# Kernel tuning notes

Hardware: AMD Instinct MI355X
Metric: run time of the kernel (lower is better)

The kernel has to match this reference:

```python
import jax, jax.numpy as jnp
import numpy as np

NUM_CAPSULE = 32
DIM_CAPSULE = 16
ROUTINGS = 3
EPS = 1e-7  # K.epsilon()


def squash(x, axis=-1):
    s2 = jnp.sum(jnp.square(x), axis=axis, keepdims=True) + EPS
    scale = jnp.sqrt(s2) / (0.5 + s2)
    return scale * x


def setup_inputs() -> dict:
    key = jax.random.key(0)
    kx, kw = jax.random.split(key)
    x = jax.random.normal(kx, (128, 2048, 128), dtype=jnp.float32)
    # glorot-uniform-scale init for (in_dim, num_capsule*dim_capsule)
    fan_in, fan_out = 128, NUM_CAPSULE * DIM_CAPSULE
    limit = np.sqrt(6.0 / (fan_in + fan_out)).astype(np.float32)
    kernel = jax.random.uniform(kw, (fan_in, fan_out), dtype=jnp.float32,
                                minval=-limit, maxval=limit)
    return {"x": x, "kernel": kernel}


def reference(x, kernel):
    B, N, _ = x.shape
    # share_weights=True: 1x1 conv1d == matmul over input_dim_capsule
    hat = jnp.einsum('bnd,dm->bnm', x, kernel)            # (B, N, C*D)
    hat = hat.reshape(B, N, NUM_CAPSULE, DIM_CAPSULE)
    hat = jnp.transpose(hat, (0, 2, 1, 3))                # (B, C, N, D)
    b = jnp.zeros(hat.shape[:3], dtype=hat.dtype)         # (B, C, N)
    o = None
    for i in range(ROUTINGS):
        c = jax.nn.softmax(b, axis=1)                     # softmax over output capsules
        o = squash(jnp.einsum('bcn,bcnd->bcd', c, hat))   # (B, C, D)
        if i < ROUTINGS - 1:
            b = jnp.einsum('bcd,bcnd->bcn', o, hat)       # agreement (replaces b, per code)
    return o
```

## Files before the change

### kernel.cpp

```cpp
#include <hip/hip_runtime.h>
#include <hip/hip_bf16.h>


#define SEQ 2048
#define KD  128

typedef __attribute__((ext_vector_type(8))) short bf16x8;
typedef __attribute__((ext_vector_type(4))) float f32x4;

__device__ __forceinline__ short f2bf(float f) {
  unsigned u = __float_as_uint(f);
  u = u + 0x7fffu + ((u >> 16) & 1u);
  return (short)(u >> 16);
}
__device__ __forceinline__ int swz(int row) {
  return ((row & 7) << 4) ^ ((row & 24) << 2);
}

__global__ __launch_bounds__(256) void prep_k(const float* __restrict__ x,
                                              short* __restrict__ xs,
                                              float* __restrict__ S) {
  int blk = blockIdx.x;
  int t = threadIdx.x, oct = t & 15, rsub = t >> 4;
  size_t row0 = (size_t)blk * 128;
  char* dst = (char*)xs + (size_t)blk * 32768;
  float sac[8] = {0.f,0.f,0.f,0.f,0.f,0.f,0.f,0.f};
  #pragma unroll
  for (int sub = 0; sub < 8; ++sub) {
    int r = sub * 16 + rsub;
    const float* gp = x + (row0 + r) * KD + oct * 8;
    float4 f0 = *(const float4*)gp, f1 = *(const float4*)(gp + 4);
    bf16x8 v; short* vp = (short*)&v;
    vp[0] = f2bf(f0.x); vp[1] = f2bf(f0.y); vp[2] = f2bf(f0.z); vp[3] = f2bf(f0.w);
    vp[4] = f2bf(f1.x); vp[5] = f2bf(f1.y); vp[6] = f2bf(f1.z); vp[7] = f2bf(f1.w);
    sac[0] += f0.x; sac[1] += f0.y; sac[2] += f0.z; sac[3] += f0.w;
    sac[4] += f1.x; sac[5] += f1.y; sac[6] += f1.z; sac[7] += f1.w;
    *(bf16x8*)(dst + ((r * 256 + oct * 16) ^ swz(r))) = v;
  }
  __shared__ float red[2048];
  float4* rp = (float4*)&red[rsub * 128 + oct * 8];
  rp[0] = make_float4(sac[0], sac[1], sac[2], sac[3]);
  rp[1] = make_float4(sac[4], sac[5], sac[6], sac[7]);
  __syncthreads();
  if (t < 128) {
    float s = 0.f;
    #pragma unroll
    for (int i = 0; i < 16; ++i) s += red[i * 128 + t];
    atomicAdd(&S[(blk >> 4) * KD + t], s);
  }
}

__global__ __launch_bounds__(64) void small_k(const float* __restrict__ W,
                                              const float* __restrict__ S,
                                              const float* __restrict__ yp,
                                              short* __restrict__ wt,
                                              float* __restrict__ out,
                                              int mode) {
  int b = blockIdx.x >> 5, c = blockIdx.x & 31;
  int l = threadIdx.x, d = l & 15, kg = l >> 4;
  const float* Wc = W + c * 16;
  float s = 0.f;
  if (mode == 0) {
    const float* Sp = S + b * KD;
    #pragma unroll 8
    for (int i = 0; i < 32; ++i) { int k = kg * 32 + i; s += Sp[k] * Wc[k * 512 + d]; }
    s *= (1.f / 32.f);
  } else {
    const float* y0 = yp + (size_t)b * 4 * 4096 + c * KD;
    #pragma unroll 8
    for (int i = 0; i < 32; ++i) {
      int k = kg * 32 + i;
      float yv = y0[k] + y0[4096 + k] + y0[8192 + k] + y0[12288 + k];
      s += yv * Wc[k * 512 + d];
    }
  }
  s += __shfl_xor(s, 16); s += __shfl_xor(s, 32);
  float s2 = s * s;
  s2 += __shfl_xor(s2, 1); s2 += __shfl_xor(s2, 2);
  s2 += __shfl_xor(s2, 4); s2 += __shfl_xor(s2, 8);
  s2 += 1e-7f;
  float o = (sqrtf(s2) / (0.5f + s2)) * s;
  if (mode == 2) { if (l < 16) out[(size_t)b * 512 + c * 16 + l] = o; return; }
  __shared__ float olds[16];
  if (l < 16) olds[l] = o;
  __syncthreads();
  #pragma unroll
  for (int h = 0; h < 2; ++h) {
    int k = l + h * 64;
    float acc = 0.f;
    #pragma unroll
    for (int dd = 0; dd < 16; ++dd) acc += olds[dd] * Wc[k * 512 + dd];
    wt[((size_t)b * 32 + c) * KD + k] = f2bf(acc);
  }
}

__global__ __launch_bounds__(256, 2) void pass_k(const short* __restrict__ xs,
                                                 const short* __restrict__ wt,
                                                 float* __restrict__ yout) {
  __shared__ char ldsbuf[49152];
  char* lx  = ldsbuf;
  char* lw  = ldsbuf + 32768;
  char* lcn = ldsbuf + 40960;
  float* yred = (float*)ldsbuf;

  int b = blockIdx.x >> 2;
  int t = threadIdx.x;
  int wv = t >> 6, lane = t & 63, l15 = lane & 15, lg = lane >> 4;

  {
    int e = t * 16, c = e >> 7, k = e & 127;
    const short* gw = wt + (size_t)b * 4096 + e;
    bf16x8 w0 = *(const bf16x8*)gw;
    bf16x8 w1 = *(const bf16x8*)(gw + 8);
    int sw = (c & 7) << 4;
    *(bf16x8*)(lw + ((c * 256 + k * 2) ^ sw)) = w0;
    *(bf16x8*)(lw + ((c * 256 + (k + 8) * 2) ^ sw)) = w1;
  }

  f32x4 zz = {0.f, 0.f, 0.f, 0.f};
  f32x4 yacc[2][8];
  #pragma unroll
  for (int i = 0; i < 2; ++i)
    #pragma unroll
    for (int j = 0; j < 8; ++j) yacc[i][j] = zz;

  for (int chunk = 0; chunk < 4; ++chunk) {
    {
      const char* gs = (const char*)xs + ((size_t)blockIdx.x * 4 + chunk) * 32768;
      #pragma unroll
      for (int sub = 0; sub < 8; ++sub) {
        int off = sub * 4096 + t * 16;
        *(bf16x8*)(lx + off) = *(const bf16x8*)(gs + off);
      }
    }
    __syncthreads();

    f32x4 sc[2][2];
    sc[0][0] = zz; sc[0][1] = zz; sc[1][0] = zz; sc[1][1] = zz;
    #pragma unroll
    for (int ks = 0; ks < 4; ++ks) {
      bf16x8 a[2], bw[2];
      #pragma unroll
      for (int mi = 0; mi < 2; ++mi) {
        int row = wv * 32 + mi * 16 + l15;
        a[mi] = *(const bf16x8*)(lx + ((row * 256 + ks * 64 + lg * 16) ^ swz(row)));
      }
      #pragma unroll
      for (int ct = 0; ct < 2; ++ct) {
        int cc = ct * 16 + l15;
        bw[ct] = *(const bf16x8*)(lw + ((cc * 256 + ks * 64 + lg * 16) ^ ((cc & 7) << 4)));
      }
      #pragma unroll
      for (int mi = 0; mi < 2; ++mi)
        #pragma unroll
        for (int ct = 0; ct < 2; ++ct)
          sc[mi][ct] = __builtin_amdgcn_mfma_f32_16x16x32_bf16(a[mi], bw[ct], sc[mi][ct], 0, 0, 0);
    }

    #pragma unroll
    for (int mi = 0; mi < 2; ++mi) {
      #pragma unroll
      for (int r = 0; r < 4; ++r) {
        float v0 = sc[mi][0][r], v1 = sc[mi][1][r];
        float mx = fmaxf(v0, v1);
        mx = fmaxf(mx, __shfl_xor(mx, 1));
        mx = fmaxf(mx, __shfl_xor(mx, 2));
        mx = fmaxf(mx, __shfl_xor(mx, 4));
        mx = fmaxf(mx, __shfl_xor(mx, 8));
        float e0 = __expf(v0 - mx), e1 = __expf(v1 - mx);
        float sm = e0 + e1;
        sm += __shfl_xor(sm, 1); sm += __shfl_xor(sm, 2);
        sm += __shfl_xor(sm, 4); sm += __shfl_xor(sm, 8);
        float inv = 1.f / sm;
        int row = wv * 32 + mi * 16 + lg * 4 + r;
        int c0 = l15, c1 = 16 + l15;
        *(short*)(lcn + ((c0 * 256 + row * 2) ^ ((c0 & 7) << 4))) = f2bf(e0 * inv);
        *(short*)(lcn + ((c1 * 256 + row * 2) ^ ((c1 & 7) << 4))) = f2bf(e1 * inv);
      }
    }
    __syncthreads();

    {
      bf16x8 a2[2];
      #pragma unroll
      for (int m2 = 0; m2 < 2; ++m2) {
        int cc = m2 * 16 + l15;
        a2[m2] = *(const bf16x8*)(lcn + ((cc * 256 + wv * 64 + lg * 16) ^ ((cc & 7) << 4)));
      }
      #pragma unroll
      for (int nt = 0; nt < 8; ++nt) {
        bf16x8 bx;
        short* bp = (short*)&bx;
        int col = nt * 16 + l15;
        int rbase = wv * 32 + lg * 8;
        #pragma unroll
        for (int j = 0; j < 8; ++j) {
          int row = rbase + j;
          bp[j] = *(const short*)(lx + ((row * 256 + col * 2) ^ swz(row)));
        }
        yacc[0][nt] = __builtin_amdgcn_mfma_f32_16x16x32_bf16(a2[0], bx, yacc[0][nt], 0, 0, 0);
        yacc[1][nt] = __builtin_amdgcn_mfma_f32_16x16x32_bf16(a2[1], bx, yacc[1][nt], 0, 0, 0);
      }
    }
    __syncthreads();
  }

  #pragma unroll 1
  for (int round = 0; round < 4; ++round) {
    if (wv == round) {
      #pragma unroll
      for (int m2 = 0; m2 < 2; ++m2)
        #pragma unroll
        for (int nt = 0; nt < 8; ++nt)
          #pragma unroll
          for (int r = 0; r < 4; ++r) {
            int cc = m2 * 16 + lg * 4 + r;
            int kk = nt * 16 + l15;
            if (round == 0) yred[cc * 128 + kk]  = yacc[m2][nt][r];
            else            yred[cc * 128 + kk] += yacc[m2][nt][r];
          }
    }
    __syncthreads();
  }
  float* yo = yout + (size_t)blockIdx.x * 4096;
  #pragma unroll
  for (int i = 0; i < 16; ++i) yo[i * 256 + t] = yred[i * 256 + t];
}

extern "C" void kernel_launch(void* const* d_in, const int* in_sizes, int n_in,
                              void* d_out, int out_size, void* d_ws, size_t ws_size,
                              hipStream_t stream) {
  const float* x = (const float*)d_in[0];
  const float* W = (const float*)d_in[1];
  float* out = (float*)d_out;
  char* ws = (char*)d_ws;
  float* S  = (float*)ws;
  float* y1 = (float*)(ws + 65536);
  float* y2 = (float*)(ws + 65536 + 8388608);
  short* wt = (short*)(ws + 65536 + 16777216);
  short* xs = (short*)(ws + 20971520);

  hipMemsetAsync(S, 0, 65536, stream);

  prep_k <<<dim3(2048), dim3(256), 0, stream>>>(x, xs, S);
  small_k<<<dim3(4096), dim3(64), 0, stream>>>(W, S, nullptr, wt, nullptr, 0);
  pass_k <<<dim3(512), dim3(256), 0, stream>>>(xs, wt, y1);
  small_k<<<dim3(4096), dim3(64), 0, stream>>>(W, nullptr, y1, wt, nullptr, 1);
  pass_k <<<dim3(512), dim3(256), 0, stream>>>(xs, wt, y2);
  small_k<<<dim3(4096), dim3(64), 0, stream>>>(W, nullptr, y2, nullptr, out, 2);
}
```

Measured before the change: 299.6 us.

## Fuse per-batch routing update into pass kernel and drop atomics and memset

The small per-(batch,capsule) kernels that computed the squashed capsule output and its projection onto W are folded into the prologue of the pass kernel. Each pass block now recomputes s, squash, and the bf16 weight tile itself. prep_k writes per-block partial sums instead of using atomics, which removes the memset. This cuts two launches and a global round-trip for wt, but it duplicates the work four times, since four blocks share each batch, and it adds serial fp32 W-loads to the front of the MFMA kernel.

```diff
diff --git a/kernel.cpp b/kernel.cpp
--- a/kernel.cpp
+++ b/kernel.cpp
@@ -19,7 +19,7 @@
 
 __global__ __launch_bounds__(256) void prep_k(const float* __restrict__ x,
                                               short* __restrict__ xs,
-                                              float* __restrict__ S) {
+                                              float* __restrict__ Sp) {
   int blk = blockIdx.x;
   int t = threadIdx.x, oct = t & 15, rsub = t >> 4;
   size_t row0 = (size_t)blk * 128;
@@ -46,76 +46,78 @@
     float s = 0.f;
     #pragma unroll
     for (int i = 0; i < 16; ++i) s += red[i * 128 + t];
-    atomicAdd(&S[(blk >> 4) * KD + t], s);
-  }
-}
-
-__global__ __launch_bounds__(64) void small_k(const float* __restrict__ W,
-                                              const float* __restrict__ S,
-                                              const float* __restrict__ yp,
-                                              short* __restrict__ wt,
-                                              float* __restrict__ out,
-                                              int mode) {
-  int b = blockIdx.x >> 5, c = blockIdx.x & 31;
-  int l = threadIdx.x, d = l & 15, kg = l >> 4;
-  const float* Wc = W + c * 16;
-  float s = 0.f;
-  if (mode == 0) {
-    const float* Sp = S + b * KD;
-    #pragma unroll 8
-    for (int i = 0; i < 32; ++i) { int k = kg * 32 + i; s += Sp[k] * Wc[k * 512 + d]; }
-    s *= (1.f / 32.f);
-  } else {
-    const float* y0 = yp + (size_t)b * 4 * 4096 + c * KD;
-    #pragma unroll 8
-    for (int i = 0; i < 32; ++i) {
-      int k = kg * 32 + i;
-      float yv = y0[k] + y0[4096 + k] + y0[8192 + k] + y0[12288 + k];
-      s += yv * Wc[k * 512 + d];
-    }
-  }
-  s += __shfl_xor(s, 16); s += __shfl_xor(s, 32);
-  float s2 = s * s;
-  s2 += __shfl_xor(s2, 1); s2 += __shfl_xor(s2, 2);
-  s2 += __shfl_xor(s2, 4); s2 += __shfl_xor(s2, 8);
-  s2 += 1e-7f;
-  float o = (sqrtf(s2) / (0.5f + s2)) * s;
-  if (mode == 2) { if (l < 16) out[(size_t)b * 512 + c * 16 + l] = o; return; }
-  __shared__ float olds[16];
-  if (l < 16) olds[l] = o;
-  __syncthreads();
-  #pragma unroll
-  for (int h = 0; h < 2; ++h) {
-    int k = l + h * 64;
-    float acc = 0.f;
-    #pragma unroll
-    for (int dd = 0; dd < 16; ++dd) acc += olds[dd] * Wc[k * 512 + dd];
-    wt[((size_t)b * 32 + c) * KD + k] = f2bf(acc);
+    Sp[blk * KD + t] = s;
   }
 }
 
 __global__ __launch_bounds__(256, 2) void pass_k(const short* __restrict__ xs,
-                                                 const short* __restrict__ wt,
-                                                 float* __restrict__ yout) {
+                                                 const float* __restrict__ W,
+                                                 const float* __restrict__ Sp,
+                                                 const float* __restrict__ ypin,
+                                                 float* __restrict__ yout,
+                                                 int iter0) {
   __shared__ char ldsbuf[49152];
   char* lx  = ldsbuf;
   char* lw  = ldsbuf + 32768;
   char* lcn = ldsbuf + 40960;
+  float* yv   = (float*)ldsbuf;
+  float* sarr = (float*)(ldsbuf + 16384);
+  float* olds = (float*)(ldsbuf + 18432);
   float* yred = (float*)ldsbuf;
 
   int b = blockIdx.x >> 2;
   int t = threadIdx.x;
   int wv = t >> 6, lane = t & 63, l15 = lane & 15, lg = lane >> 4;
 
-  {
-    int e = t * 16, c = e >> 7, k = e & 127;
-    const short* gw = wt + (size_t)b * 4096 + e;
-    bf16x8 w0 = *(const bf16x8*)gw;
-    bf16x8 w1 = *(const bf16x8*)(gw + 8);
-    int sw = (c & 7) << 4;
-    *(bf16x8*)(lw + ((c * 256 + k * 2) ^ sw)) = w0;
-    *(bf16x8*)(lw + ((c * 256 + (k + 8) * 2) ^ sw)) = w1;
-  }
+  if (iter0) {
+    if (t < 128) {
+      float s = 0.f;
+      #pragma unroll
+      for (int j = 0; j < 16; ++j) s += Sp[(b * 16 + j) * KD + t];
+      sarr[t] = s * (1.f / 32.f);
+    }
+    __syncthreads();
+    #pragma unroll
+    for (int i = 0; i < 16; ++i) { int idx = i * 256 + t; yv[idx] = sarr[idx & 127]; }
+  } else {
+    const float* y0 = ypin + (size_t)b * 4 * 4096;
+    #pragma unroll
+    for (int i = 0; i < 16; ++i) {
+      int idx = i * 256 + t;
+      yv[idx] = y0[idx] + y0[4096 + idx] + y0[8192 + idx] + y0[12288 + idx];
+    }
+  }
+  __syncthreads();
+  float sreg[2];
+  #pragma unroll
+  for (int h = 0; h < 2; ++h) {
+    int cd = h * 256 + t, c = cd >> 4, d = cd & 15;
+    float acc = 0.f;
+    #pragma unroll 8
+    for (int k = 0; k < KD; ++k) acc += yv[c * KD + k] * W[k * 512 + c * 16 + d];
+    sreg[h] = acc;
+  }
+  __syncthreads();
+  sarr[t] = sreg[0]; sarr[256 + t] = sreg[1];
+  __syncthreads();
+  #pragma unroll
+  for (int h = 0; h < 2; ++h) {
+    int cd = h * 256 + t, c = cd >> 4;
+    float s2 = 1e-7f;
+    #pragma unroll
+    for (int dd = 0; dd < 16; ++dd) { float v = sarr[c * 16 + dd]; s2 += v * v; }
+    olds[cd] = (sqrtf(s2) / (0.5f + s2)) * sreg[h];
+  }
+  __syncthreads();
+  #pragma unroll
+  for (int i = 0; i < 16; ++i) {
+    int idx = i * 256 + t, c = idx >> 7, k = idx & 127;
+    float acc = 0.f;
+    #pragma unroll
+    for (int dd = 0; dd < 16; ++dd) acc += olds[c * 16 + dd] * W[k * 512 + c * 16 + dd];
+    *(short*)(lw + ((c * 256 + k * 2) ^ ((c & 7) << 4))) = f2bf(acc);
+  }
+  __syncthreads();
 
   f32x4 zz = {0.f, 0.f, 0.f, 0.f};
   f32x4 yacc[2][8];
@@ -227,6 +229,29 @@
   for (int i = 0; i < 16; ++i) yo[i * 256 + t] = yred[i * 256 + t];
 }
 
+__global__ __launch_bounds__(64) void out_k(const float* __restrict__ W,
+                                            const float* __restrict__ yp,
+                                            float* __restrict__ out) {
+  int b = blockIdx.x >> 5, c = blockIdx.x & 31;
+  int l = threadIdx.x, d = l & 15, kg = l >> 4;
+  const float* Wc = W + c * 16;
+  const float* y0 = yp + (size_t)b * 4 * 4096 + c * KD;
+  float s = 0.f;
+  #pragma unroll 8
+  for (int i = 0; i < 32; ++i) {
+    int k = kg * 32 + i;
+    float yvv = y0[k] + y0[4096 + k] + y0[8192 + k] + y0[12288 + k];
+    s += yvv * Wc[k * 512 + d];
+  }
+  s += __shfl_xor(s, 16); s += __shfl_xor(s, 32);
+  float s2 = s * s;
+  s2 += __shfl_xor(s2, 1); s2 += __shfl_xor(s2, 2);
+  s2 += __shfl_xor(s2, 4); s2 += __shfl_xor(s2, 8);
+  s2 += 1e-7f;
+  float o = (sqrtf(s2) / (0.5f + s2)) * s;
+  if (l < 16) out[(size_t)b * 512 + c * 16 + l] = o;
+}
+
 extern "C" void kernel_launch(void* const* d_in, const int* in_sizes, int n_in,
                               void* d_out, int out_size, void* d_ws, size_t ws_size,
                               hipStream_t stream) {
@@ -234,18 +259,13 @@
   const float* W = (const float*)d_in[1];
   float* out = (float*)d_out;
   char* ws = (char*)d_ws;
-  float* S  = (float*)ws;
-  float* y1 = (float*)(ws + 65536);
-  float* y2 = (float*)(ws + 65536 + 8388608);
-  short* wt = (short*)(ws + 65536 + 16777216);
-  short* xs = (short*)(ws + 20971520);
-
-  hipMemsetAsync(S, 0, 65536, stream);
-
-  prep_k <<<dim3(2048), dim3(256), 0, stream>>>(x, xs, S);
-  small_k<<<dim3(4096), dim3(64), 0, stream>>>(W, S, nullptr, wt, nullptr, 0);
-  pass_k <<<dim3(512), dim3(256), 0, stream>>>(xs, wt, y1);
-  small_k<<<dim3(4096), dim3(64), 0, stream>>>(W, nullptr, y1, wt, nullptr, 1);
-  pass_k <<<dim3(512), dim3(256), 0, stream>>>(xs, wt, y2);
-  small_k<<<dim3(4096), dim3(64), 0, stream>>>(W, nullptr, y2, nullptr, out, 2);
-}
+  float* Sp = (float*)ws;
+  float* y1 = (float*)(ws + (1u << 20));
+  float* y2 = (float*)(ws + 9u * (1u << 20));
+  short* xs = (short*)(ws + 17u * (1u << 20));
+
+  prep_k<<<dim3(2048), dim3(256), 0, stream>>>(x, xs, Sp);
+  pass_k<<<dim3(512), dim3(256), 0, stream>>>(xs, W, Sp, nullptr, y1, 1);
+  pass_k<<<dim3(512), dim3(256), 0, stream>>>(xs, W, nullptr, y1, y2, 0);
+  out_k <<<dim3(4096), dim3(64), 0, stream>>>(W, y2, out);
+}
```

Result: slower. 332.3 us (+10.9%).
